# Kernel optimization log

Measured on AMD Instinct MI355X. Metric: run time of the kernel, lower is better.

Reference implementation:

```python
import jax, jax.numpy as jnp
import numpy as np

NUM_SENTENCES = 32
MAX_SENT_LEN = 64
EMBED_DIM = 768
BATCH = 16
TEXT_LEN = NUM_SENTENCES * MAX_SENT_LEN  # 2048


def setup_inputs() -> dict:
    key = jax.random.key(0)
    k1, k2 = jax.random.split(key)
    inputs = jax.random.normal(k1, (BATCH, TEXT_LEN, EMBED_DIM), dtype=jnp.float32)
    W = jax.random.normal(k2, (EMBED_DIM, 2 * NUM_SENTENCES), dtype=jnp.float32) * 0.02
    b = jnp.zeros((2 * NUM_SENTENCES,), dtype=jnp.float32)
    return {"inputs": inputs, "W": W, "b": b}


def reference(inputs, W, b):
    B, T, E = inputs.shape
    S, L = NUM_SENTENCES, MAX_SENT_LEN

    # offsets from mean-pooled input through Dense(2*S)
    pooled = jnp.mean(inputs, axis=1)                      # [B, E]
    offsets = pooled @ W + b                               # [B, 2S]
    # clip to [0, L-1], cast (truncation == floor for nonneg values)
    start_off = jnp.clip(offsets[:, :S], 0.0, float(L - 1)).astype(jnp.int32)  # [B, S]
    end_off = jnp.clip(offsets[:, S:], 0.0, float(L - 1)).astype(jnp.int32)    # [B, S]

    base = (jnp.arange(S, dtype=jnp.int32) * L)[None, :]   # [1, S]
    start_idx = jnp.clip(base + start_off, 0, T - L)        # [B, S]
    end_idx = jnp.clip(base + L + end_off, start_idx, T)    # [B, S]

    # vectorized slice+pad: position j of sentence i comes from start_idx+j,
    # valid while j < (end_idx - start_idx) and j < L (pad/truncate to L)
    j = jnp.arange(L, dtype=jnp.int32)                      # [L]
    gather_idx = start_idx[:, :, None] + j[None, None, :]   # [B, S, L]
    valid = j[None, None, :] < (end_idx - start_idx)[:, :, None]  # [B, S, L]

    flat_idx = jnp.clip(gather_idx, 0, T - 1).reshape(B, S * L)
    gathered = jnp.take_along_axis(inputs, flat_idx[:, :, None], axis=1)
    gathered = gathered.reshape(B, S, L, E)
    out = jnp.where(valid[:, :, :, None], gathered, jnp.zeros((), inputs.dtype))
    return out
```

## Files before the change

### kernel.cpp

```cpp
#include <hip/hip_runtime.h>

#define BATCH 16
#define T_LEN 2048
#define E_DIM 768
#define E4 (E_DIM / 4)
#define N_SENT 32
#define S_LEN 64
#define NCHUNK 32
#define ROWS_PER_CHUNK (T_LEN / NCHUNK)

__global__ void pool_partial(const float4* __restrict__ in4, float4* __restrict__ partial4) {
    const int tx = threadIdx.x;
    const int b  = blockIdx.x;
    const int tc = blockIdx.y;
    const float4* p = in4 + ((size_t)b * T_LEN + (size_t)tc * ROWS_PER_CHUNK) * E4 + tx;
    float4 s = make_float4(0.f, 0.f, 0.f, 0.f);
#pragma unroll 8
    for (int t = 0; t < ROWS_PER_CHUNK; ++t) {
        float4 v = p[(size_t)t * E4];
        s.x += v.x; s.y += v.y; s.z += v.z; s.w += v.w;
    }
    partial4[((size_t)tc * BATCH + b) * E4 + tx] = s;
}

__global__ void compute_idx(const float4* __restrict__ partial4,
                            const float* __restrict__ W,
                            const float* __restrict__ bias,
                            int* __restrict__ sidx, int* __restrict__ eidx) {
    __shared__ float pooled[E_DIM];
    __shared__ float colsum[4][2 * N_SENT];
    __shared__ int   offi[2 * N_SENT];
    const int b   = blockIdx.x;
    const int tid = threadIdx.x;

    if (tid < E4) {
        float4 s = make_float4(0.f, 0.f, 0.f, 0.f);
#pragma unroll
        for (int tc = 0; tc < NCHUNK; ++tc) {
            float4 v = partial4[((size_t)tc * BATCH + b) * E4 + tid];
            s.x += v.x; s.y += v.y; s.z += v.z; s.w += v.w;
        }
        const float inv = 1.0f / (float)T_LEN;
        ((float4*)pooled)[tid] = make_float4(s.x * inv, s.y * inv, s.z * inv, s.w * inv);
    }
    __syncthreads();

    const int c = tid & 63;
    const int q = tid >> 6;
    float acc = 0.f;
    const float* pb = pooled + q * 192;
    const float* Wq = W + (size_t)q * 192 * (2 * N_SENT) + c;
#pragma unroll 8
    for (int e = 0; e < 192; ++e) acc += pb[e] * Wq[(size_t)e * (2 * N_SENT)];
    colsum[q][c] = acc;
    __syncthreads();

    if (tid < 2 * N_SENT) {
        float o = bias[tid] + colsum[0][tid] + colsum[1][tid] + colsum[2][tid] + colsum[3][tid];
        float cl = fminf(fmaxf(o, 0.f), (float)(S_LEN - 1));
        offi[tid] = (int)cl;
    }
    __syncthreads();

    if (tid < N_SENT) {
        const int so   = offi[tid];
        const int eo   = offi[N_SENT + tid];
        const int base = tid * S_LEN;
        int si = min(base + so, T_LEN - S_LEN);
        int ei = min(max(base + S_LEN + eo, si), T_LEN);
        sidx[b * N_SENT + tid] = si;
        eidx[b * N_SENT + tid] = ei;
    }
}

__global__ void gather_rows(const float4* __restrict__ in4,
                            const int* __restrict__ sidx,
                            const int* __restrict__ eidx,
                            float4* __restrict__ out4) {
    const int row = blockIdx.x * 4 + threadIdx.y;
    const int j = row & (S_LEN - 1);
    const int s = (row >> 6) & (N_SENT - 1);
    const int b = row >> 11;
    const int si = sidx[b * N_SENT + s];
    const int ei = eidx[b * N_SENT + s];
    float4 v = make_float4(0.f, 0.f, 0.f, 0.f);
    if (j < ei - si) {
        v = in4[((size_t)b * T_LEN + (si + j)) * E4 + threadIdx.x];
    }
    out4[(size_t)row * E4 + threadIdx.x] = v;
}

extern "C" void kernel_launch(void* const* d_in, const int* in_sizes, int n_in,
                              void* d_out, int out_size, void* d_ws, size_t ws_size,
                              hipStream_t stream) {
    const float4* in4 = (const float4*)d_in[0];
    const float*  W   = (const float*)d_in[1];
    const float*  bias= (const float*)d_in[2];
    float4* out4 = (float4*)d_out;

    float4* partial4 = (float4*)d_ws;
    int* sidx = (int*)((char*)d_ws + (size_t)NCHUNK * BATCH * E4 * sizeof(float4));
    int* eidx = sidx + BATCH * N_SENT;

    pool_partial<<<dim3(BATCH, NCHUNK), 192, 0, stream>>>(in4, partial4);
    compute_idx<<<BATCH, 256, 0, stream>>>(partial4, W, bias, sidx, eidx);
    gather_rows<<<dim3(BATCH * N_SENT * S_LEN / 4), dim3(192, 4), 0, stream>>>(
        in4, sidx, eidx, (float4*)out4);
}
```

Baseline: 205.5 us.

## Fuse pooling, offset computation and gather into one cooperative kernel

Replaces three kernel launches with a single cooperative kernel of 512 blocks that uses grid-wide syncs between the pooling, index computation and gather phases. Each block pools a 64-row chunk with 256 threads and a shared-memory reduction, and later copies the matching sentence slice, so the chunk it read may still be in cache. The aim is to drop launch overhead and the gaps between kernels. In exchange it adds two grid.sync barriers, and during the middle phase only 16 blocks do any work.

```diff
diff --git a/kernel.cpp b/kernel.cpp
--- a/kernel.cpp
+++ b/kernel.cpp
@@ -1,4 +1,7 @@
 #include <hip/hip_runtime.h>
+#include <hip/hip_cooperative_groups.h>
+
+namespace cg = cooperative_groups;
 
 #define BATCH 16
 #define T_LEN 2048
@@ -7,103 +10,134 @@
 #define N_SENT 32
 #define S_LEN 64
 #define NCHUNK 32
-#define ROWS_PER_CHUNK (T_LEN / NCHUNK)
+#define NBLK (BATCH * NCHUNK)
 
-__global__ void pool_partial(const float4* __restrict__ in4, float4* __restrict__ partial4) {
-    const int tx = threadIdx.x;
-    const int b  = blockIdx.x;
-    const int tc = blockIdx.y;
-    const float4* p = in4 + ((size_t)b * T_LEN + (size_t)tc * ROWS_PER_CHUNK) * E4 + tx;
-    float4 s = make_float4(0.f, 0.f, 0.f, 0.f);
-#pragma unroll 8
-    for (int t = 0; t < ROWS_PER_CHUNK; ++t) {
-        float4 v = p[(size_t)t * E4];
-        s.x += v.x; s.y += v.y; s.z += v.z; s.w += v.w;
-    }
-    partial4[((size_t)tc * BATCH + b) * E4 + tx] = s;
+__device__ __forceinline__ void add4(float4& a, const float4 v) {
+    a.x += v.x; a.y += v.y; a.z += v.z; a.w += v.w;
 }
 
-__global__ void compute_idx(const float4* __restrict__ partial4,
-                            const float* __restrict__ W,
-                            const float* __restrict__ bias,
-                            int* __restrict__ sidx, int* __restrict__ eidx) {
-    __shared__ float pooled[E_DIM];
-    __shared__ float colsum[4][2 * N_SENT];
-    __shared__ int   offi[2 * N_SENT];
-    const int b   = blockIdx.x;
-    const int tid = threadIdx.x;
+__global__ __launch_bounds__(256, 2) void fused_all(
+    const float4* __restrict__ in4,
+    const float*  __restrict__ W,
+    const float*  __restrict__ bias,
+    float4* __restrict__ partial4,
+    int* __restrict__ sidx,
+    int* __restrict__ eidx,
+    float4* __restrict__ out4)
+{
+    cg::grid_group grid = cg::this_grid();
 
-    if (tid < E4) {
-        float4 s = make_float4(0.f, 0.f, 0.f, 0.f);
-#pragma unroll
-        for (int tc = 0; tc < NCHUNK; ++tc) {
-            float4 v = partial4[((size_t)tc * BATCH + b) * E4 + tid];
-            s.x += v.x; s.y += v.y; s.z += v.z; s.w += v.w;
+    const int tid  = threadIdx.x;
+    const int lane = tid & 63;
+    const int q    = tid >> 6;
+    const int g    = blockIdx.x;
+    const int b    = g >> 5;
+    const int tc   = g & 31;
+
+    __shared__ float4 red[4][E4];
+
+    {
+        const float4* base = in4 + ((size_t)b * T_LEN + (size_t)tc * 64) * E4;
+        float4 s0 = make_float4(0.f,0.f,0.f,0.f), s1 = s0, s2 = s0;
+        #pragma unroll 4
+        for (int k = 0; k < 16; ++k) {
+            const float4* p = base + (size_t)(q * 16 + k) * E4 + lane;
+            add4(s0, p[0]);
+            add4(s1, p[64]);
+            add4(s2, p[128]);
         }
-        const float inv = 1.0f / (float)T_LEN;
-        ((float4*)pooled)[tid] = make_float4(s.x * inv, s.y * inv, s.z * inv, s.w * inv);
+        red[q][lane]       = s0;
+        red[q][lane + 64]  = s1;
+        red[q][lane + 128] = s2;
     }
     __syncthreads();
+    if (tid < E4) {
+        float4 t = red[0][tid];
+        add4(t, red[1][tid]); add4(t, red[2][tid]); add4(t, red[3][tid]);
+        partial4[((size_t)tc * BATCH + b) * E4 + tid] = t;
+    }
+    grid.sync();
 
-    const int c = tid & 63;
-    const int q = tid >> 6;
-    float acc = 0.f;
-    const float* pb = pooled + q * 192;
-    const float* Wq = W + (size_t)q * 192 * (2 * N_SENT) + c;
-#pragma unroll 8
-    for (int e = 0; e < 192; ++e) acc += pb[e] * Wq[(size_t)e * (2 * N_SENT)];
-    colsum[q][c] = acc;
-    __syncthreads();
+    if (g < BATCH) {
+        __shared__ float pooled[E_DIM];
+        __shared__ float colsum[4][2 * N_SENT];
+        __shared__ int   offi[2 * N_SENT];
 
-    if (tid < 2 * N_SENT) {
-        float o = bias[tid] + colsum[0][tid] + colsum[1][tid] + colsum[2][tid] + colsum[3][tid];
-        float cl = fminf(fmaxf(o, 0.f), (float)(S_LEN - 1));
-        offi[tid] = (int)cl;
+        if (tid < E4) {
+            float4 s = make_float4(0.f,0.f,0.f,0.f);
+            #pragma unroll
+            for (int pc = 0; pc < NCHUNK; ++pc)
+                add4(s, partial4[((size_t)pc * BATCH + g) * E4 + tid]);
+            const float inv = 1.0f / (float)T_LEN;
+            ((float4*)pooled)[tid] = make_float4(s.x*inv, s.y*inv, s.z*inv, s.w*inv);
+        }
+        __syncthreads();
+
+        const int c  = tid & 63;
+        const int qq = tid >> 6;
+        float acc = 0.f;
+        const float* pb = pooled + qq * 192;
+        const float* Wq = W + (size_t)qq * 192 * (2 * N_SENT) + c;
+        #pragma unroll 8
+        for (int e = 0; e < 192; ++e) acc += pb[e] * Wq[(size_t)e * (2 * N_SENT)];
+        colsum[qq][c] = acc;
+        __syncthreads();
+
+        if (tid < 2 * N_SENT) {
+            float o = bias[tid] + colsum[0][tid] + colsum[1][tid]
+                                + colsum[2][tid] + colsum[3][tid];
+            float cl = fminf(fmaxf(o, 0.f), (float)(S_LEN - 1));
+            offi[tid] = (int)cl;
+        }
+        __syncthreads();
+
+        if (tid < N_SENT) {
+            const int so   = offi[tid];
+            const int eo   = offi[N_SENT + tid];
+            const int bse  = tid * S_LEN;
+            int si = min(bse + so, T_LEN - S_LEN);
+            int ei = min(max(bse + S_LEN + eo, si), T_LEN);
+            sidx[g * N_SENT + tid] = si;
+            eidx[g * N_SENT + tid] = ei;
+        }
     }
-    __syncthreads();
+    grid.sync();
 
-    if (tid < N_SENT) {
-        const int so   = offi[tid];
-        const int eo   = offi[N_SENT + tid];
-        const int base = tid * S_LEN;
-        int si = min(base + so, T_LEN - S_LEN);
-        int ei = min(max(base + S_LEN + eo, si), T_LEN);
-        sidx[b * N_SENT + tid] = si;
-        eidx[b * N_SENT + tid] = ei;
+    {
+        const int si  = sidx[b * N_SENT + tc];
+        const int ei  = eidx[b * N_SENT + tc];
+        const int len = ei - si;
+        const float4* src = in4  + ((size_t)b * T_LEN + si) * E4 + lane;
+        float4*       dst = out4 + (((size_t)b * N_SENT + tc) * S_LEN) * E4 + lane;
+        const float4 z = make_float4(0.f,0.f,0.f,0.f);
+        #pragma unroll 2
+        for (int k = 0; k < 16; ++k) {
+            const int j = q * 16 + k;
+            float4 v0 = z, v1 = z, v2 = z;
+            if (j < len) {
+                const float4* sp = src + (size_t)j * E4;
+                v0 = sp[0]; v1 = sp[64]; v2 = sp[128];
+            }
+            float4* dp = dst + (size_t)j * E4;
+            dp[0] = v0; dp[64] = v1; dp[128] = v2;
+        }
     }
-}
-
-__global__ void gather_rows(const float4* __restrict__ in4,
-                            const int* __restrict__ sidx,
-                            const int* __restrict__ eidx,
-                            float4* __restrict__ out4) {
-    const int row = blockIdx.x * 4 + threadIdx.y;
-    const int j = row & (S_LEN - 1);
-    const int s = (row >> 6) & (N_SENT - 1);
-    const int b = row >> 11;
-    const int si = sidx[b * N_SENT + s];
-    const int ei = eidx[b * N_SENT + s];
-    float4 v = make_float4(0.f, 0.f, 0.f, 0.f);
-    if (j < ei - si) {
-        v = in4[((size_t)b * T_LEN + (si + j)) * E4 + threadIdx.x];
-    }
-    out4[(size_t)row * E4 + threadIdx.x] = v;
 }
 
 extern "C" void kernel_launch(void* const* d_in, const int* in_sizes, int n_in,
                               void* d_out, int out_size, void* d_ws, size_t ws_size,
                               hipStream_t stream) {
-    const float4* in4 = (const float4*)d_in[0];
-    const float*  W   = (const float*)d_in[1];
-    const float*  bias= (const float*)d_in[2];
+    const float4* in4  = (const float4*)d_in[0];
+    const float*  W    = (const float*)d_in[1];
+    const float*  bias = (const float*)d_in[2];
     float4* out4 = (float4*)d_out;
 
     float4* partial4 = (float4*)d_ws;
     int* sidx = (int*)((char*)d_ws + (size_t)NCHUNK * BATCH * E4 * sizeof(float4));
     int* eidx = sidx + BATCH * N_SENT;
 
-    pool_partial<<<dim3(BATCH, NCHUNK), 192, 0, stream>>>(in4, partial4);
-    compute_idx<<<BATCH, 256, 0, stream>>>(partial4, W, bias, sidx, eidx);
-    gather_rows<<<dim3(BATCH * N_SENT * S_LEN / 4), dim3(192, 4), 0, stream>>>(
-        in4, sidx, eidx, (float4*)out4);
+    void* args[] = { (void*)&in4, (void*)&W, (void*)&bias, (void*)&partial4,
+                     (void*)&sidx, (void*)&eidx, (void*)&out4 };
+    hipLaunchCooperativeKernel((const void*)fused_all, dim3(NBLK), dim3(256),
+                               args, 0, stream);
 }
```

After: 322.1 us. 56.7% more time.

## Restructure gather to per-sentence blocks with nontemporal stores; double pool chunks

Applied to the files above, without the earlier changes.

The gather kernel now assigns each 256-thread block half a sentence (32 rows). Each wave copies 8 rows, with every lane moving three float4s per row, and the bounds are read once per block. Output writes use nontemporal stores so the streaming output does not pollute the cache. The pooling stage doubles its chunk count to 64 for more parallelism across the input, in exchange for a larger partial-sum reduction in compute_idx. The workspace grows to hold twice as many partials.

```diff
diff --git a/kernel.cpp b/kernel.cpp
--- a/kernel.cpp
+++ b/kernel.cpp
@@ -6,8 +6,10 @@
 #define E4 (E_DIM / 4)
 #define N_SENT 32
 #define S_LEN 64
-#define NCHUNK 32
+#define NCHUNK 64
 #define ROWS_PER_CHUNK (T_LEN / NCHUNK)
+
+typedef float nf4 __attribute__((ext_vector_type(4)));
 
 __global__ void pool_partial(const float4* __restrict__ in4, float4* __restrict__ partial4) {
     const int tx = threadIdx.x;
@@ -35,7 +37,7 @@
 
     if (tid < E4) {
         float4 s = make_float4(0.f, 0.f, 0.f, 0.f);
-#pragma unroll
+#pragma unroll 8
         for (int tc = 0; tc < NCHUNK; ++tc) {
             float4 v = partial4[((size_t)tc * BATCH + b) * E4 + tid];
             s.x += v.x; s.y += v.y; s.z += v.z; s.w += v.w;
@@ -73,21 +75,38 @@
     }
 }
 
-__global__ void gather_rows(const float4* __restrict__ in4,
-                            const int* __restrict__ sidx,
-                            const int* __restrict__ eidx,
-                            float4* __restrict__ out4) {
-    const int row = blockIdx.x * 4 + threadIdx.y;
-    const int j = row & (S_LEN - 1);
-    const int s = (row >> 6) & (N_SENT - 1);
-    const int b = row >> 11;
-    const int si = sidx[b * N_SENT + s];
-    const int ei = eidx[b * N_SENT + s];
-    float4 v = make_float4(0.f, 0.f, 0.f, 0.f);
-    if (j < ei - si) {
-        v = in4[((size_t)b * T_LEN + (si + j)) * E4 + threadIdx.x];
+__global__ __launch_bounds__(256) void gather_rows(const float4* __restrict__ in4,
+                                                   const int* __restrict__ sidx,
+                                                   const int* __restrict__ eidx,
+                                                   float4* __restrict__ out4) {
+    const int blk  = blockIdx.x;
+    const int half = blk & 1;
+    const int s    = (blk >> 1) & (N_SENT - 1);
+    const int b    = blk >> 6;
+    const int lane = threadIdx.x & 63;
+    const int q    = threadIdx.x >> 6;
+
+    const int si  = sidx[b * N_SENT + s];
+    const int ei  = eidx[b * N_SENT + s];
+    const int len = ei - si;
+
+    const float4* src = in4  + ((size_t)b * T_LEN + si) * E4 + lane;
+    float4*       dst = out4 + (((size_t)b * N_SENT + s) * S_LEN) * E4 + lane;
+    const float4 z = make_float4(0.f, 0.f, 0.f, 0.f);
+
+#pragma unroll 4
+    for (int k = 0; k < 8; ++k) {
+        const int j = half * 32 + q * 8 + k;
+        float4 v0 = z, v1 = z, v2 = z;
+        if (j < len) {
+            const float4* sp = src + (size_t)j * E4;
+            v0 = sp[0]; v1 = sp[64]; v2 = sp[128];
+        }
+        nf4* dp = (nf4*)(dst + (size_t)j * E4);
+        __builtin_nontemporal_store(*(const nf4*)&v0, dp);
+        __builtin_nontemporal_store(*(const nf4*)&v1, dp + 64);
+        __builtin_nontemporal_store(*(const nf4*)&v2, dp + 128);
     }
-    out4[(size_t)row * E4 + threadIdx.x] = v;
 }
 
 extern "C" void kernel_launch(void* const* d_in, const int* in_sizes, int n_in,
@@ -104,6 +123,5 @@
 
     pool_partial<<<dim3(BATCH, NCHUNK), 192, 0, stream>>>(in4, partial4);
     compute_idx<<<BATCH, 256, 0, stream>>>(partial4, W, bias, sidx, eidx);
-    gather_rows<<<dim3(BATCH * N_SENT * S_LEN / 4), dim3(192, 4), 0, stream>>>(
-        in4, sidx, eidx, (float4*)out4);
+    gather_rows<<<dim3(BATCH * N_SENT * 2), 256, 0, stream>>>(in4, sidx, eidx, out4);
 }
```

After: 208.0 us. About the same (+1.2%).
